# Kernel tuning notes

Measured on AMD Instinct MI355X. Metric: run time of the kernel, lower is better.

Reference implementation:

```python
import jax, jax.numpy as jnp
import numpy as np
from jax import lax

RATES = (2, 3, 5, 9)
C_IN = 64
B, H, W = 4, 128, 128


def conv2d(x, w, b, dilation):
    # x: [B,C,H,W], w: [O,I,3,3]; padding=dilation keeps spatial size
    y = lax.conv_general_dilated(
        x, w, window_strides=(1, 1),
        padding=[(dilation, dilation), (dilation, dilation)],
        rhs_dilation=(dilation, dilation),
        dimension_numbers=('NCHW', 'OIHW', 'NCHW'))
    return y + b[None, :, None, None]


def bilinear_sample(x, py, px):
    # x: [B,C,H,W]; py,px: [B,K,H,W] float sampling positions; zeros outside
    Hh, Ww = x.shape[-2], x.shape[-1]
    y0 = jnp.floor(py)
    x0 = jnp.floor(px)
    wy1 = py - y0
    wx1 = px - x0
    wy0 = 1.0 - wy1
    wx0 = 1.0 - wx1

    def gather(yi, xi):
        valid = (yi >= 0) & (yi < Hh) & (xi >= 0) & (xi < Ww)
        yc = jnp.clip(yi, 0, Hh - 1).astype(jnp.int32)
        xc = jnp.clip(xi, 0, Ww - 1).astype(jnp.int32)
        # per-batch fancy gather: [C,K,H,W]
        vals = jax.vmap(lambda im, yy, xx: im[:, yy, xx])(x, yc, xc)
        return vals * valid[:, None].astype(x.dtype)

    out = (gather(y0, x0) * (wy0 * wx0)[:, None]
           + gather(y0, x0 + 1) * (wy0 * wx1)[:, None]
           + gather(y0 + 1, x0) * (wy1 * wx0)[:, None]
           + gather(y0 + 1, x0 + 1) * (wy1 * wx1)[:, None])
    return out  # [B,C,K,H,W]


def deform_conv(x, offset, weight, dilation):
    # offset: [B,18,H,W] = (dy,dx) per kernel point; weight: [O,C,3,3]
    b, c, h, w = x.shape
    K = 9
    off = offset.reshape(b, K, 2, h, w)
    dy, dx = off[:, :, 0], off[:, :, 1]
    ky = jnp.repeat((jnp.arange(3) - 1) * dilation, 3).astype(x.dtype)  # [9]
    kx = jnp.tile((jnp.arange(3) - 1) * dilation, 3).astype(x.dtype)
    hh = jnp.arange(h, dtype=x.dtype)[None, None, :, None]
    ww = jnp.arange(w, dtype=x.dtype)[None, None, None, :]
    py = hh + ky[None, :, None, None] + dy
    px = ww + kx[None, :, None, None] + dx
    sampled = bilinear_sample(x, py, px)  # [B,C,K,H,W]
    w9 = weight.reshape(weight.shape[0], c, K)
    return jnp.einsum('bckhw,ock->bohw', sampled, w9)


def setup_inputs() -> dict:
    key = jax.random.key(0)
    ks = jax.random.split(key, 8)
    s = 0.05
    return {
        'x': jax.random.normal(ks[0], (B, C_IN, H, W), jnp.float32),
        'dw': jax.random.normal(ks[1], (4, C_IN, C_IN, 3, 3), jnp.float32) * s,
        'ow': jax.random.normal(ks[2], (4, 18, C_IN, 3, 3), jnp.float32) * s,
        'ob': jax.random.normal(ks[3], (4, 18), jnp.float32) * s,
        'se_w1': jax.random.normal(ks[4], (C_IN, 4 * C_IN), jnp.float32) * s,
        'se_b1': jax.random.normal(ks[5], (C_IN,), jnp.float32) * s,
        'se_w2': jax.random.normal(ks[6], (4 * C_IN, C_IN), jnp.float32) * s,
        'se_b2': jax.random.normal(ks[7], (4 * C_IN,), jnp.float32) * s,
    }


def reference(x, dw, ow, ob, se_w1, se_b1, se_w2, se_b2):
    b, c, h, w = x.shape
    outs = []
    for i in range(4):
        j = (i - 1) % 4  # faithful to `self.offsets[i - 1]` in the source
        off = jax.nn.relu(conv2d(x, ow[j], ob[j], RATES[j]))
        outs.append(deform_conv(x, off, dw[i], RATES[i]))
    cat = jnp.concatenate(outs, axis=1)  # [B,4C,H,W]
    # SENet on concatenated features
    g = cat.mean(axis=(2, 3))  # [B,4C]
    h1 = jax.nn.relu(g @ se_w1.T + se_b1)
    s = jax.nn.sigmoid(h1 @ se_w2.T + se_b2)  # [B,4C]
    gated = (1.0 + s)[:, :, None, None] * cat
    fused = gated.reshape(b, 4, c, h, w).sum(axis=1)  # sum over the 4 stages
    return x + fused
```

## Files before the change

### kernel.cpp

```cpp
#include <hip/hip_runtime.h>
#include <hip/hip_bf16.h>
#include <math.h>

#define BATCH 4
#define CIN 64
#define HH 128
#define WW 128
#define HWP (HH*WW)

#define OFF_OFF   0
#define CAT_OFF   4718592
#define XHWC_OFF  (CAT_OFF + 8388608)
#define WTH_OFF   (XHWC_OFF + 2097152)
#define OWH_OFF   (WTH_OFF + 73728)
#define G_OFF     (OWH_OFF + 36864)
#define SCALE_OFF (G_OFF + 1024)

typedef _Float16 h16x2 __attribute__((ext_vector_type(2)));
typedef _Float16 h16x8 __attribute__((ext_vector_type(8)));
typedef float    f32x4 __attribute__((ext_vector_type(4)));

union h8view { h16x8 v8; h16x2 v2[4]; };

__device__ __forceinline__ int rate_of(int i) {
    return (i == 0) ? 2 : (i == 1) ? 3 : (i == 2) ? 5 : 9;
}

__global__ __launch_bounds__(256) void prep_kernel(
    const float* __restrict__ dw, const float* __restrict__ ow,
    _Float16* __restrict__ wth, _Float16* __restrict__ owh)
{
    int idx = blockIdx.x * 256 + threadIdx.x;
    if (idx < 147456) {
        int c = idx & 63;
        int k = (idx >> 6) % 9;
        int r = idx / 576;
        int o = r & 63;
        int i = r >> 6;
        wth[idx] = (_Float16)dw[((i * 64 + o) * 64 + c) * 9 + k];
        return;
    }
    int idx2 = idx - 147456;
    if (idx2 < 73728) {
        int c = idx2 & 63;
        int r = idx2 >> 6;
        int o = r & 31;
        int r2 = r >> 5;
        int tap = r2 % 9;
        int j = r2 / 9;
        owh[idx2] = (o < 18) ? (_Float16)ow[((j * 18 + o) * 64 + c) * 9 + tap]
                             : (_Float16)0.f;
    }
}

__global__ __launch_bounds__(256) void xhwc_kernel(
    const float* __restrict__ x, _Float16* __restrict__ xhwc)
{
    const int t  = threadIdx.x;
    const int b  = blockIdx.y;
    const int p0 = blockIdx.x * 64;
    const int px = t & 63;
    const int cO = t >> 6;

    const float* xb = x + (size_t)b * CIN * HWP + p0 + px;
    _Float16* xh = xhwc + ((size_t)b * HWP + p0 + px) * 64;

#pragma unroll
    for (int g = 0; g < 2; ++g) {
        const int cb = cO * 8 + g * 32;
        h16x8 v;
#pragma unroll
        for (int cj = 0; cj < 8; ++cj)
            v[cj] = (_Float16)xb[(size_t)(cb + cj) * HWP];
        *(h16x8*)(xh + cb) = v;
    }
}

__global__ __launch_bounds__(256) void offset_mfma_kernel(
    const _Float16* __restrict__ xhwc, const _Float16* __restrict__ owh,
    const float* __restrict__ ob, float* __restrict__ off)
{
    __shared__ __align__(16) _Float16 S2[64][72];

    const int t  = threadIdx.x;
    const int z  = blockIdx.y;
    const int j  = z >> 2, b = z & 3;
    const int d  = rate_of(j);
    const int p0 = blockIdx.x * 64;
    const int ph = p0 >> 7;
    const int cb0 = p0 & 127;

    const int wv = t >> 6, lane = t & 63;
    const int nl = lane & 15, quad = lane >> 4;

    const _Float16* xh = xhwc + (size_t)b * HWP * 64;

    f32x4 acc[2];
    acc[0] = (f32x4){0.f, 0.f, 0.f, 0.f};
    acc[1] = (f32x4){0.f, 0.f, 0.f, 0.f};

    for (int k = 0; k < 9; ++k) {
        const int iy = k / 3, ix = k % 3;
        const int ys = ph + (iy - 1) * d;
        const bool rowok = (unsigned)ys < (unsigned)HH;

        if (k) __syncthreads();

#pragma unroll
        for (int q = 0; q < 2; ++q) {
            const int task = q * 256 + t;
            const int px = task >> 3, chunk = task & 7;
            const int xs = cb0 + px + (ix - 1) * d;
            h16x8 v = {};
            if (rowok && (unsigned)xs < (unsigned)WW)
                v = *(const h16x8*)(xh + ((size_t)(ys * WW + xs)) * 64 + chunk * 8);
            *(h16x8*)&S2[px][chunk * 8] = v;
        }
        __syncthreads();

#pragma unroll
        for (int q2 = 0; q2 < 2; ++q2) {
            h16x8 a = *(const h16x8*)&S2[wv * 16 + nl][q2 * 32 + quad * 8];
#pragma unroll
            for (int nt = 0; nt < 2; ++nt) {
                const _Float16* brow = owh
                    + ((size_t)((j * 9 + k) * 32 + nt * 16 + nl)) * 64;
                h16x8 bf = *(const h16x8*)&brow[q2 * 32 + quad * 8];
                acc[nt] = __builtin_amdgcn_mfma_f32_16x16x32_f16(a, bf, acc[nt], 0, 0, 0);
            }
        }
    }

    float* op = off + (size_t)z * 18 * HWP + p0;
#pragma unroll
    for (int nt = 0; nt < 2; ++nt) {
        const int o = nt * 16 + nl;
        if (o < 18) {
            const float bias = ob[j * 18 + o];
#pragma unroll
            for (int r = 0; r < 4; ++r) {
                const int pxl = wv * 16 + quad * 4 + r;
                op[(size_t)o * HWP + pxl] = fmaxf(acc[nt][r] + bias, 0.f);
            }
        }
    }
}

__global__ __launch_bounds__(256) void deform_mfma_kernel(
    const _Float16* __restrict__ xhwc, const _Float16* __restrict__ wth,
    const float* __restrict__ off, _Float16* __restrict__ cat)
{
    __shared__ __align__(16) _Float16 S[128][72];

    const int t  = threadIdx.x;
    const int z  = blockIdx.y;
    const int i  = z >> 2, b = z & 3;
    const int d  = rate_of(i);
    const int j  = (i + 3) & 3;
    const int ty = blockIdx.x >> 1;
    const int tx = blockIdx.x & 1;

    const int chunk = t & 7;
    const int pxb   = t >> 3;

    const int wv = t >> 6, lane = t & 63;
    const int nl = lane & 15, quad = lane >> 4;

    const _Float16* xh = xhwc + (size_t)b * HWP * 64;
    const float* offb = off + ((size_t)(j * 4 + b) * 18) * HWP;

    f32x4 acc[8];
#pragma unroll
    for (int a = 0; a < 8; ++a) acc[a] = (f32x4){0.f, 0.f, 0.f, 0.f};

    for (int k = 0; k < 9; ++k) {
        const int iy = k / 3, ix = k % 3;

        if (k) __syncthreads();

#pragma unroll
        for (int it = 0; it < 4; ++it) {
            const int psub = it * 32 + pxb;
            const int sly = psub >> 6, slx = psub & 63;
            const int ph = ty * 2 + sly, pw = tx * 64 + slx;
            const int pg = ph * WW + pw;

            float dy = offb[(2 * k) * HWP + pg];
            float dx = offb[(2 * k + 1) * HWP + pg];
            float py = (float)(ph + (iy - 1) * d) + dy;
            float px = (float)(pw + (ix - 1) * d) + dx;
            float fy0 = floorf(py), fx0 = floorf(px);
            float wy1 = py - fy0, wx1 = px - fx0;
            float wy0 = 1.f - wy1, wx0 = 1.f - wx1;
            int y0 = (int)fy0, x0 = (int)fx0;
            int y1 = y0 + 1,  x1 = x0 + 1;
            bool vy0 = (unsigned)y0 < (unsigned)HH, vy1 = (unsigned)y1 < (unsigned)HH;
            bool vx0 = (unsigned)x0 < (unsigned)WW, vx1 = (unsigned)x1 < (unsigned)WW;
            int yc0 = min(max(y0, 0), HH - 1), yc1 = min(max(y1, 0), HH - 1);
            int xc0 = min(max(x0, 0), WW - 1), xc1 = min(max(x1, 0), WW - 1);
            float w00 = (vy0 && vx0) ? wy0 * wx0 : 0.f;
            float w01 = (vy0 && vx1) ? wy0 * wx1 : 0.f;
            float w10 = (vy1 && vx0) ? wy1 * wx0 : 0.f;
            float w11 = (vy1 && vx1) ? wy1 * wx1 : 0.f;

            const _Float16 h00 = (_Float16)w00, h01 = (_Float16)w01;
            const _Float16 h10 = (_Float16)w10, h11 = (_Float16)w11;
            const h16x2 w00p = {h00, h00}, w01p = {h01, h01};
            const h16x2 w10p = {h10, h10}, w11p = {h11, h11};

            const int cb = chunk * 8;
            h8view u00, u01, u10, u11, outv;
            u00.v8 = *(const h16x8*)(xh + (size_t)(yc0 * WW + xc0) * 64 + cb);
            u01.v8 = *(const h16x8*)(xh + (size_t)(yc0 * WW + xc1) * 64 + cb);
            u10.v8 = *(const h16x8*)(xh + (size_t)(yc1 * WW + xc0) * 64 + cb);
            u11.v8 = *(const h16x8*)(xh + (size_t)(yc1 * WW + xc1) * 64 + cb);
#pragma unroll
            for (int pp = 0; pp < 4; ++pp) {
                h16x2 r = u00.v2[pp] * w00p + u01.v2[pp] * w01p
                        + u10.v2[pp] * w10p + u11.v2[pp] * w11p;
                outv.v2[pp] = r;
            }
            *(h16x8*)&S[psub][cb] = outv.v8;
        }
        __syncthreads();

#pragma unroll
        for (int q2 = 0; q2 < 2; ++q2) {
            h16x8 b0 = *(const h16x8*)&S[wv * 32 + nl][q2 * 32 + quad * 8];
            h16x8 b1 = *(const h16x8*)&S[wv * 32 + 16 + nl][q2 * 32 + quad * 8];
#pragma unroll
            for (int mt = 0; mt < 4; ++mt) {
                const _Float16* wrow = wth
                    + ((size_t)((i * 64 + mt * 16 + nl) * 9 + k)) * 64;
                h16x8 a = *(const h16x8*)&wrow[q2 * 32 + quad * 8];
                acc[mt * 2 + 0] = __builtin_amdgcn_mfma_f32_16x16x32_f16(a, b0, acc[mt * 2 + 0], 0, 0, 0);
                acc[mt * 2 + 1] = __builtin_amdgcn_mfma_f32_16x16x32_f16(a, b1, acc[mt * 2 + 1], 0, 0, 0);
            }
        }
    }

#pragma unroll
    for (int mt = 0; mt < 4; ++mt) {
#pragma unroll
        for (int nt = 0; nt < 2; ++nt) {
            const int psub = wv * 32 + nt * 16 + nl;
            const int prow = ty * 2 + (psub >> 6);
            const int pcol = tx * 64 + (psub & 63);
            _Float16* cp = cat
                + ((size_t)(b * 256 + i * 64 + mt * 16 + quad * 4)) * HWP
                + prow * WW + pcol;
            const f32x4 v = acc[mt * 2 + nt];
#pragma unroll
            for (int r = 0; r < 4; ++r)
                cp[(size_t)r * HWP] = (_Float16)v[r];
        }
    }
}

__global__ __launch_bounds__(256) void reduce_kernel(
    const _Float16* __restrict__ cat, float* __restrict__ g)
{
    const int bc = blockIdx.x;
    const _Float16* p = cat + (size_t)bc * HWP;
    float s = 0.f;
#pragma unroll
    for (int q = 0; q < 8; ++q) {
        h16x8 v8 = *(const h16x8*)(p + q * 2048 + threadIdx.x * 8);
#pragma unroll
        for (int e = 0; e < 8; ++e) s += (float)v8[e];
    }
#pragma unroll
    for (int o = 32; o > 0; o >>= 1) s += __shfl_down(s, o, 64);
    __shared__ float ls[4];
    if ((threadIdx.x & 63) == 0) ls[threadIdx.x >> 6] = s;
    __syncthreads();
    if (threadIdx.x == 0) {
        g[bc] = (ls[0] + ls[1] + ls[2] + ls[3]) * (1.f / (float)HWP);
    }
}

__global__ __launch_bounds__(256) void se_kernel(
    const float* __restrict__ g,  const float* __restrict__ w1,
    const float* __restrict__ b1, const float* __restrict__ w2,
    const float* __restrict__ b2, float* __restrict__ scale)
{
    __shared__ float gs[1024];
    __shared__ float h1s[256];
    const int t = threadIdx.x;
#pragma unroll
    for (int q = 0; q < 4; ++q) gs[q * 256 + t] = g[q * 256 + t];
    __syncthreads();
    {
        int b = t >> 6, o = t & 63;
        float a = b1[o];
        for (int c = 0; c < 256; ++c)
            a = fmaf(gs[b * 256 + c], w1[o * 256 + c], a);
        h1s[t] = fmaxf(a, 0.f);
    }
    __syncthreads();
#pragma unroll
    for (int q = 0; q < 4; ++q) {
        int idx = q * 256 + t;
        int b = idx >> 8, cc = idx & 255;
        float a = b2[cc];
#pragma unroll 8
        for (int o = 0; o < 64; ++o)
            a = fmaf(h1s[b * 64 + o], w2[cc * 64 + o], a);
        scale[idx] = 1.f + 1.f / (1.f + expf(-a));
    }
}

__global__ __launch_bounds__(256) void final_kernel(
    const float* __restrict__ x, const _Float16* __restrict__ cat,
    const float* __restrict__ scale, float* __restrict__ out)
{
    const int gid = blockIdx.x;
    const int p = (gid & 63) * 256 + threadIdx.x;
    const int c = (gid >> 6) & 63;
    const int b = gid >> 12;
    const float s0 = scale[b * 256 + c];
    const float s1 = scale[b * 256 + 64 + c];
    const float s2 = scale[b * 256 + 128 + c];
    const float s3 = scale[b * 256 + 192 + c];
    const _Float16* cb = cat + ((size_t)(b * 256 + c)) * HWP + p;
    float v = x[(size_t)(b * 64 + c) * HWP + p];
    v = fmaf(s0, (float)cb[0 * 64 * HWP], v);
    v = fmaf(s1, (float)cb[1 * 64 * HWP], v);
    v = fmaf(s2, (float)cb[2 * 64 * HWP], v);
    v = fmaf(s3, (float)cb[3 * 64 * HWP], v);
    out[(size_t)(b * 64 + c) * HWP + p] = v;
}

extern "C" void kernel_launch(void* const* d_in, const int* in_sizes, int n_in,
                              void* d_out, int out_size, void* d_ws, size_t ws_size,
                              hipStream_t stream) {
    const float* x  = (const float*)d_in[0];
    const float* dw = (const float*)d_in[1];
    const float* ow = (const float*)d_in[2];
    const float* ob = (const float*)d_in[3];
    const float* w1 = (const float*)d_in[4];
    const float* b1 = (const float*)d_in[5];
    const float* w2 = (const float*)d_in[6];
    const float* b2 = (const float*)d_in[7];
    float* out = (float*)d_out;
    float* ws  = (float*)d_ws;

    float* OFF      = ws + OFF_OFF;
    _Float16* CAT   = (_Float16*)(ws + CAT_OFF);
    _Float16* XHWC  = (_Float16*)(ws + XHWC_OFF);
    _Float16* WTH   = (_Float16*)(ws + WTH_OFF);
    _Float16* OWH   = (_Float16*)(ws + OWH_OFF);
    float* G        = ws + G_OFF;
    float* SCALE    = ws + SCALE_OFF;

    prep_kernel<<<864, 256, 0, stream>>>(dw, ow, WTH, OWH);
    xhwc_kernel<<<dim3(256, 4), 256, 0, stream>>>(x, XHWC);
    offset_mfma_kernel<<<dim3(256, 16), 256, 0, stream>>>(XHWC, OWH, ob, OFF);
    deform_mfma_kernel<<<dim3(128, 16), 256, 0, stream>>>(XHWC, WTH, OFF, CAT);
    reduce_kernel<<<1024, 256, 0, stream>>>(CAT, G);
    se_kernel<<<1, 256, 0, stream>>>(G, w1, b1, w2, b2, SCALE);
    final_kernel<<<16384, 256, 0, stream>>>(x, CAT, SCALE, out);
}
```

Measured before the change: 312.9 us.

## Double-buffer LDS staging in offset and deform MFMA kernels with register prefetch

Both the offset convolution kernel and the deformable convolution kernel now use two LDS buffers. The global loads (or bilinear gathers) for the next kernel tap are issued into registers before the MFMA work on the current tap and written to the other buffer afterwards, leaving one barrier per tap instead of two. The deform kernel also prefetches offsets two taps ahead and hoists the pixel index math. This is meant to hide gather latency behind MFMA, at the cost of doubled LDS and many more live registers (16 h16x8 values plus weights), which may reduce occupancy or cause spills.

```diff
diff --git a/kernel.cpp b/kernel.cpp
--- a/kernel.cpp
+++ b/kernel.cpp
@@ -80,7 +80,7 @@
     const _Float16* __restrict__ xhwc, const _Float16* __restrict__ owh,
     const float* __restrict__ ob, float* __restrict__ off)
 {
-    __shared__ __align__(16) _Float16 S2[64][72];
+    __shared__ __align__(16) _Float16 S2[2][64][72];
 
     const int t  = threadIdx.x;
     const int z  = blockIdx.y;
@@ -99,28 +99,42 @@
     acc[0] = (f32x4){0.f, 0.f, 0.f, 0.f};
     acc[1] = (f32x4){0.f, 0.f, 0.f, 0.f};
 
-    for (int k = 0; k < 9; ++k) {
-        const int iy = k / 3, ix = k % 3;
+    h16x8 v[2];
+
+    auto stage_load = [&](int kk) {
+        const int iy = kk / 3, ix = kk % 3;
         const int ys = ph + (iy - 1) * d;
         const bool rowok = (unsigned)ys < (unsigned)HH;
-
-        if (k) __syncthreads();
-
 #pragma unroll
         for (int q = 0; q < 2; ++q) {
             const int task = q * 256 + t;
-            const int px = task >> 3, chunk = task & 7;
+            const int px = task >> 3, ch = task & 7;
             const int xs = cb0 + px + (ix - 1) * d;
-            h16x8 v = {};
+            h16x8 vv = {};
             if (rowok && (unsigned)xs < (unsigned)WW)
-                v = *(const h16x8*)(xh + ((size_t)(ys * WW + xs)) * 64 + chunk * 8);
-            *(h16x8*)&S2[px][chunk * 8] = v;
-        }
-        __syncthreads();
+                vv = *(const h16x8*)(xh + ((size_t)(ys * WW + xs)) * 64 + ch * 8);
+            v[q] = vv;
+        }
+    };
+    auto stage_store = [&](int buf) {
+#pragma unroll
+        for (int q = 0; q < 2; ++q) {
+            const int task = q * 256 + t;
+            const int px = task >> 3, ch = task & 7;
+            *(h16x8*)&S2[buf][px][ch * 8] = v[q];
+        }
+    };
+
+    stage_load(0);
+    stage_store(0);
+    __syncthreads();
+
+    for (int k = 0; k < 9; ++k) {
+        if (k < 8) stage_load(k + 1);
 
 #pragma unroll
         for (int q2 = 0; q2 < 2; ++q2) {
-            h16x8 a = *(const h16x8*)&S2[wv * 16 + nl][q2 * 32 + quad * 8];
+            h16x8 a = *(const h16x8*)&S2[k & 1][wv * 16 + nl][q2 * 32 + quad * 8];
 #pragma unroll
             for (int nt = 0; nt < 2; ++nt) {
                 const _Float16* brow = owh
@@ -129,6 +143,9 @@
                 acc[nt] = __builtin_amdgcn_mfma_f32_16x16x32_f16(a, bf, acc[nt], 0, 0, 0);
             }
         }
+
+        if (k < 8) stage_store((k + 1) & 1);
+        __syncthreads();
     }
 
     float* op = off + (size_t)z * 18 * HWP + p0;
@@ -150,7 +167,7 @@
     const _Float16* __restrict__ xhwc, const _Float16* __restrict__ wth,
     const float* __restrict__ off, _Float16* __restrict__ cat)
 {
-    __shared__ __align__(16) _Float16 S[128][72];
+    __shared__ __align__(16) _Float16 S[2][128][72];
 
     const int t  = threadIdx.x;
     const int z  = blockIdx.y;
@@ -162,6 +179,7 @@
 
     const int chunk = t & 7;
     const int pxb   = t >> 3;
+    const int cb    = chunk * 8;
 
     const int wv = t >> 6, lane = t & 63;
     const int nl = lane & 15, quad = lane >> 4;
@@ -169,26 +187,30 @@
     const _Float16* xh = xhwc + (size_t)b * HWP * 64;
     const float* offb = off + ((size_t)(j * 4 + b) * 18) * HWP;
 
+    int phv[4], pwv[4], pgv[4];
+#pragma unroll
+    for (int it = 0; it < 4; ++it) {
+        const int psub = it * 32 + pxb;
+        phv[it] = ty * 2 + (psub >> 6);
+        pwv[it] = tx * 64 + (psub & 63);
+        pgv[it] = phv[it] * WW + pwv[it];
+    }
+
     f32x4 acc[8];
 #pragma unroll
     for (int a = 0; a < 8; ++a) acc[a] = (f32x4){0.f, 0.f, 0.f, 0.f};
 
-    for (int k = 0; k < 9; ++k) {
-        const int iy = k / 3, ix = k % 3;
-
-        if (k) __syncthreads();
-
+    h8view u[4][4];
+    h16x2  wp[4][4];
+    float  ocy[4], ocx[4];
+    float  ony[4], onx[4];
+
+    auto gather = [&](int kk) {
+        const int iy = kk / 3, ix = kk % 3;
 #pragma unroll
         for (int it = 0; it < 4; ++it) {
-            const int psub = it * 32 + pxb;
-            const int sly = psub >> 6, slx = psub & 63;
-            const int ph = ty * 2 + sly, pw = tx * 64 + slx;
-            const int pg = ph * WW + pw;
-
-            float dy = offb[(2 * k) * HWP + pg];
-            float dx = offb[(2 * k + 1) * HWP + pg];
-            float py = (float)(ph + (iy - 1) * d) + dy;
-            float px = (float)(pw + (ix - 1) * d) + dx;
+            float py = (float)(phv[it] + (iy - 1) * d) + ocy[it];
+            float px = (float)(pwv[it] + (ix - 1) * d) + ocx[it];
             float fy0 = floorf(py), fx0 = floorf(px);
             float wy1 = py - fy0, wx1 = px - fx0;
             float wy0 = 1.f - wy1, wx0 = 1.f - wx1;
@@ -202,32 +224,61 @@
             float w01 = (vy0 && vx1) ? wy0 * wx1 : 0.f;
             float w10 = (vy1 && vx0) ? wy1 * wx0 : 0.f;
             float w11 = (vy1 && vx1) ? wy1 * wx1 : 0.f;
-
             const _Float16 h00 = (_Float16)w00, h01 = (_Float16)w01;
             const _Float16 h10 = (_Float16)w10, h11 = (_Float16)w11;
-            const h16x2 w00p = {h00, h00}, w01p = {h01, h01};
-            const h16x2 w10p = {h10, h10}, w11p = {h11, h11};
-
-            const int cb = chunk * 8;
-            h8view u00, u01, u10, u11, outv;
-            u00.v8 = *(const h16x8*)(xh + (size_t)(yc0 * WW + xc0) * 64 + cb);
-            u01.v8 = *(const h16x8*)(xh + (size_t)(yc0 * WW + xc1) * 64 + cb);
-            u10.v8 = *(const h16x8*)(xh + (size_t)(yc1 * WW + xc0) * 64 + cb);
-            u11.v8 = *(const h16x8*)(xh + (size_t)(yc1 * WW + xc1) * 64 + cb);
-#pragma unroll
-            for (int pp = 0; pp < 4; ++pp) {
-                h16x2 r = u00.v2[pp] * w00p + u01.v2[pp] * w01p
-                        + u10.v2[pp] * w10p + u11.v2[pp] * w11p;
-                outv.v2[pp] = r;
+            wp[it][0] = (h16x2){h00, h00};
+            wp[it][1] = (h16x2){h01, h01};
+            wp[it][2] = (h16x2){h10, h10};
+            wp[it][3] = (h16x2){h11, h11};
+            u[it][0].v8 = *(const h16x8*)(xh + (size_t)(yc0 * WW + xc0) * 64 + cb);
+            u[it][1].v8 = *(const h16x8*)(xh + (size_t)(yc0 * WW + xc1) * 64 + cb);
+            u[it][2].v8 = *(const h16x8*)(xh + (size_t)(yc1 * WW + xc0) * 64 + cb);
+            u[it][3].v8 = *(const h16x8*)(xh + (size_t)(yc1 * WW + xc1) * 64 + cb);
+        }
+    };
+
+    auto blendstore = [&](int buf) {
+#pragma unroll
+        for (int it = 0; it < 4; ++it) {
+            h8view outv;
+#pragma unroll
+            for (int pp = 0; pp < 4; ++pp)
+                outv.v2[pp] = u[it][0].v2[pp] * wp[it][0] + u[it][1].v2[pp] * wp[it][1]
+                            + u[it][2].v2[pp] * wp[it][2] + u[it][3].v2[pp] * wp[it][3];
+            *(h16x8*)&S[buf][it * 32 + pxb][cb] = outv.v8;
+        }
+    };
+
+#pragma unroll
+    for (int it = 0; it < 4; ++it) {
+        ocy[it] = offb[0 * HWP + pgv[it]];
+        ocx[it] = offb[1 * HWP + pgv[it]];
+    }
+    gather(0);
+    blendstore(0);
+#pragma unroll
+    for (int it = 0; it < 4; ++it) {
+        ocy[it] = offb[2 * HWP + pgv[it]];
+        ocx[it] = offb[3 * HWP + pgv[it]];
+    }
+    __syncthreads();
+
+    for (int k = 0; k < 9; ++k) {
+        if (k < 8) {
+            gather(k + 1);
+            if (k < 7) {
+#pragma unroll
+                for (int it = 0; it < 4; ++it) {
+                    ony[it] = offb[(2 * (k + 2)) * HWP + pgv[it]];
+                    onx[it] = offb[(2 * (k + 2) + 1) * HWP + pgv[it]];
+                }
             }
-            *(h16x8*)&S[psub][cb] = outv.v8;
-        }
-        __syncthreads();
+        }
 
 #pragma unroll
         for (int q2 = 0; q2 < 2; ++q2) {
-            h16x8 b0 = *(const h16x8*)&S[wv * 32 + nl][q2 * 32 + quad * 8];
-            h16x8 b1 = *(const h16x8*)&S[wv * 32 + 16 + nl][q2 * 32 + quad * 8];
+            h16x8 b0 = *(const h16x8*)&S[k & 1][wv * 32 + nl][q2 * 32 + quad * 8];
+            h16x8 b1 = *(const h16x8*)&S[k & 1][wv * 32 + 16 + nl][q2 * 32 + quad * 8];
 #pragma unroll
             for (int mt = 0; mt < 4; ++mt) {
                 const _Float16* wrow = wth
@@ -237,6 +288,13 @@
                 acc[mt * 2 + 1] = __builtin_amdgcn_mfma_f32_16x16x32_f16(a, b1, acc[mt * 2 + 1], 0, 0, 0);
             }
         }
+
+        if (k < 8) {
+            blendstore((k + 1) & 1);
+#pragma unroll
+            for (int it = 0; it < 4; ++it) { ocy[it] = ony[it]; ocx[it] = onx[it]; }
+        }
+        __syncthreads();
     }
 
 #pragma unroll
```

After: 305.4 us. -2.4%, faster.

## Merge prep kernels, stage offset-conv row halos, store offsets as fp16, fuse pooling

Applied to the files above, without the earlier changes.

Merges the weight-prep and NHWC conversion kernels into one launch that also zeroes the pooling buffer. The offset convolution now stages one padded input row per kernel row in shared memory, reused by three taps with register prefetch, instead of reloading for each of nine taps. Offsets are written as interleaved fp16 (dy,dx) pairs, halving offset traffic. The separate mean-reduction kernel is removed: per-channel sums are reduced in the deform kernel and accumulated with atomics. This costs some offset precision and adds atomic contention and ordering nondeterminism.

```diff
diff --git a/kernel.cpp b/kernel.cpp
--- a/kernel.cpp
+++ b/kernel.cpp
@@ -26,61 +26,67 @@
     return (i == 0) ? 2 : (i == 1) ? 3 : (i == 2) ? 5 : 9;
 }
 
-__global__ __launch_bounds__(256) void prep_kernel(
-    const float* __restrict__ dw, const float* __restrict__ ow,
-    _Float16* __restrict__ wth, _Float16* __restrict__ owh)
-{
-    int idx = blockIdx.x * 256 + threadIdx.x;
-    if (idx < 147456) {
-        int c = idx & 63;
-        int k = (idx >> 6) % 9;
-        int r = idx / 576;
-        int o = r & 63;
-        int i = r >> 6;
-        wth[idx] = (_Float16)dw[((i * 64 + o) * 64 + c) * 9 + k];
+__global__ __launch_bounds__(256) void prep_all_kernel(
+    const float* __restrict__ x,  const float* __restrict__ dw,
+    const float* __restrict__ ow, _Float16* __restrict__ wth,
+    _Float16* __restrict__ owh,   _Float16* __restrict__ xhwc,
+    float* __restrict__ g)
+{
+    const int bx = blockIdx.x;
+    const int t  = threadIdx.x;
+
+    if (bx < 864) {
+        int idx = bx * 256 + t;
+        if (idx < 147456) {
+            int c = idx & 63;
+            int k = (idx >> 6) % 9;
+            int r = idx / 576;
+            int o = r & 63;
+            int i = r >> 6;
+            wth[idx] = (_Float16)dw[((i * 64 + o) * 64 + c) * 9 + k];
+            return;
+        }
+        int idx2 = idx - 147456;
+        if (idx2 < 73728) {
+            int c = idx2 & 63;
+            int r = idx2 >> 6;
+            int o = r & 31;
+            int r2 = r >> 5;
+            int tap = r2 % 9;
+            int j = r2 / 9;
+            owh[idx2] = (o < 18) ? (_Float16)ow[((j * 18 + o) * 64 + c) * 9 + tap]
+                                 : (_Float16)0.f;
+        }
         return;
     }
-    int idx2 = idx - 147456;
-    if (idx2 < 73728) {
-        int c = idx2 & 63;
-        int r = idx2 >> 6;
-        int o = r & 31;
-        int r2 = r >> 5;
-        int tap = r2 % 9;
-        int j = r2 / 9;
-        owh[idx2] = (o < 18) ? (_Float16)ow[((j * 18 + o) * 64 + c) * 9 + tap]
-                             : (_Float16)0.f;
-    }
-}
-
-__global__ __launch_bounds__(256) void xhwc_kernel(
-    const float* __restrict__ x, _Float16* __restrict__ xhwc)
-{
-    const int t  = threadIdx.x;
-    const int b  = blockIdx.y;
-    const int p0 = blockIdx.x * 64;
-    const int px = t & 63;
-    const int cO = t >> 6;
-
-    const float* xb = x + (size_t)b * CIN * HWP + p0 + px;
-    _Float16* xh = xhwc + ((size_t)b * HWP + p0 + px) * 64;
-
-#pragma unroll
-    for (int g = 0; g < 2; ++g) {
-        const int cb = cO * 8 + g * 32;
-        h16x8 v;
-#pragma unroll
-        for (int cj = 0; cj < 8; ++cj)
-            v[cj] = (_Float16)xb[(size_t)(cb + cj) * HWP];
-        *(h16x8*)(xh + cb) = v;
-    }
+    if (bx < 1888) {
+        const int tb = bx - 864;
+        const int b  = tb >> 8;
+        const int p0 = (tb & 255) * 64;
+        const int px = t & 63;
+        const int cO = t >> 6;
+        const float* xb = x + (size_t)b * CIN * HWP + p0 + px;
+        _Float16* xh = xhwc + ((size_t)b * HWP + p0 + px) * 64;
+#pragma unroll
+        for (int gq = 0; gq < 2; ++gq) {
+            const int cb = cO * 8 + gq * 32;
+            h16x8 v;
+#pragma unroll
+            for (int cj = 0; cj < 8; ++cj)
+                v[cj] = (_Float16)xb[(size_t)(cb + cj) * HWP];
+            *(h16x8*)(xh + cb) = v;
+        }
+        return;
+    }
+#pragma unroll
+    for (int q = 0; q < 4; ++q) g[q * 256 + t] = 0.f;
 }
 
 __global__ __launch_bounds__(256) void offset_mfma_kernel(
     const _Float16* __restrict__ xhwc, const _Float16* __restrict__ owh,
-    const float* __restrict__ ob, float* __restrict__ off)
-{
-    __shared__ __align__(16) _Float16 S2[64][72];
+    const float* __restrict__ ob, _Float16* __restrict__ offh)
+{
+    __shared__ __align__(16) _Float16 S2[82][72];
 
     const int t  = threadIdx.x;
     const int z  = blockIdx.y;
@@ -95,52 +101,83 @@
 
     const _Float16* xh = xhwc + (size_t)b * HWP * 64;
 
+    const int width = 64 + 2 * d;
+    const int ntask = width * 8;
+
     f32x4 acc[2];
     acc[0] = (f32x4){0.f, 0.f, 0.f, 0.f};
     acc[1] = (f32x4){0.f, 0.f, 0.f, 0.f};
 
-    for (int k = 0; k < 9; ++k) {
-        const int iy = k / 3, ix = k % 3;
-        const int ys = ph + (iy - 1) * d;
+    h16x8 sv[3];
+
+    auto stage_load = [&](int g) {
+        const int ys = ph + (g - 1) * d;
         const bool rowok = (unsigned)ys < (unsigned)HH;
-
-        if (k) __syncthreads();
-
-#pragma unroll
-        for (int q = 0; q < 2; ++q) {
+#pragma unroll
+        for (int q = 0; q < 3; ++q) {
             const int task = q * 256 + t;
-            const int px = task >> 3, chunk = task & 7;
-            const int xs = cb0 + px + (ix - 1) * d;
-            h16x8 v = {};
-            if (rowok && (unsigned)xs < (unsigned)WW)
-                v = *(const h16x8*)(xh + ((size_t)(ys * WW + xs)) * 64 + chunk * 8);
-            *(h16x8*)&S2[px][chunk * 8] = v;
-        }
+            h16x8 vv = {};
+            if (task < ntask) {
+                const int sp = task >> 3, ch = task & 7;
+                const int xs = cb0 - d + sp;
+                if (rowok && (unsigned)xs < (unsigned)WW)
+                    vv = *(const h16x8*)(xh + ((size_t)(ys * WW + xs)) * 64 + ch * 8);
+            }
+            sv[q] = vv;
+        }
+    };
+    auto stage_store = [&]() {
+#pragma unroll
+        for (int q = 0; q < 3; ++q) {
+            const int task = q * 256 + t;
+            if (task < ntask) {
+                const int sp = task >> 3, ch = task & 7;
+                *(h16x8*)&S2[sp][ch * 8] = sv[q];
+            }
+        }
+    };
+
+    stage_load(0);
+    stage_store();
+    __syncthreads();
+
+    for (int g = 0; g < 3; ++g) {
+        if (g < 2) stage_load(g + 1);
+
+#pragma unroll
+        for (int ix = 0; ix < 3; ++ix) {
+            const int k = g * 3 + ix;
+#pragma unroll
+            for (int q2 = 0; q2 < 2; ++q2) {
+                h16x8 a = *(const h16x8*)&S2[wv * 16 + nl + ix * d][q2 * 32 + quad * 8];
+#pragma unroll
+                for (int nt = 0; nt < 2; ++nt) {
+                    const _Float16* brow = owh
+                        + ((size_t)((j * 9 + k) * 32 + nt * 16 + nl)) * 64;
+                    h16x8 bf = *(const h16x8*)&brow[q2 * 32 + quad * 8];
+                    acc[nt] = __builtin_amdgcn_mfma_f32_16x16x32_f16(a, bf, acc[nt], 0, 0, 0);
+                }
+            }
+        }
+
         __syncthreads();
-
-#pragma unroll
-        for (int q2 = 0; q2 < 2; ++q2) {
-            h16x8 a = *(const h16x8*)&S2[wv * 16 + nl][q2 * 32 + quad * 8];
-#pragma unroll
-            for (int nt = 0; nt < 2; ++nt) {
-                const _Float16* brow = owh
-                    + ((size_t)((j * 9 + k) * 32 + nt * 16 + nl)) * 64;
-                h16x8 bf = *(const h16x8*)&brow[q2 * 32 + quad * 8];
-                acc[nt] = __builtin_amdgcn_mfma_f32_16x16x32_f16(a, bf, acc[nt], 0, 0, 0);
-            }
-        }
-    }
-
-    float* op = off + (size_t)z * 18 * HWP + p0;
+        if (g < 2) stage_store();
+        __syncthreads();
+    }
+
+    _Float16* op = offh + (size_t)z * 9 * HWP * 2;
 #pragma unroll
     for (int nt = 0; nt < 2; ++nt) {
         const int o = nt * 16 + nl;
         if (o < 18) {
             const float bias = ob[j * 18 + o];
+            const int k  = o >> 1;
+            const int lo = o & 1;
 #pragma unroll
             for (int r = 0; r < 4; ++r) {
                 const int pxl = wv * 16 + quad * 4 + r;
-                op[(size_t)o * HWP + pxl] = fmaxf(acc[nt][r] + bias, 0.f);
+                op[((size_t)k * HWP + p0 + pxl) * 2 + lo] =
+                    (_Float16)fmaxf(acc[nt][r] + bias, 0.f);
             }
         }
     }
@@ -148,7 +185,8 @@
 
 __global__ __launch_bounds__(256) void deform_mfma_kernel(
     const _Float16* __restrict__ xhwc, const _Float16* __restrict__ wth,
-    const float* __restrict__ off, _Float16* __restrict__ cat)
+    const _Float16* __restrict__ offh, _Float16* __restrict__ cat,
+    float* __restrict__ g)
 {
     __shared__ __align__(16) _Float16 S[128][72];
 
@@ -162,12 +200,13 @@
 
     const int chunk = t & 7;
     const int pxb   = t >> 3;
+    const int cb    = chunk * 8;
 
     const int wv = t >> 6, lane = t & 63;
     const int nl = lane & 15, quad = lane >> 4;
 
     const _Float16* xh = xhwc + (size_t)b * HWP * 64;
-    const float* offb = off + ((size_t)(j * 4 + b) * 18) * HWP;
+    const _Float16* offb = offh + (size_t)(j * 4 + b) * 9 * HWP * 2;
 
     f32x4 acc[8];
 #pragma unroll
@@ -185,8 +224,9 @@
             const int ph = ty * 2 + sly, pw = tx * 64 + slx;
             const int pg = ph * WW + pw;
 
-            float dy = offb[(2 * k) * HWP + pg];
-            float dx = offb[(2 * k + 1) * HWP + pg];
+            h16x2 od = *(const h16x2*)&offb[((size_t)k * HWP + pg) * 2];
+            float dy = (float)od[0];
+            float dx = (float)od[1];
             float py = (float)(ph + (iy - 1) * d) + dy;
             float px = (float)(pw + (ix - 1) * d) + dx;
             float fy0 = floorf(py), fx0 = floorf(px);
@@ -208,7 +248,6 @@
             const h16x2 w00p = {h00, h00}, w01p = {h01, h01};
             const h16x2 w10p = {h10, h10}, w11p = {h11, h11};
 
-            const int cb = chunk * 8;
             h8view u00, u01, u10, u11, outv;
             u00.v8 = *(const h16x8*)(xh + (size_t)(yc0 * WW + xc0) * 64 + cb);
             u01.v8 = *(const h16x8*)(xh + (size_t)(yc0 * WW + xc1) * 64 + cb);
@@ -255,27 +294,18 @@
                 cp[(size_t)r * HWP] = (_Float16)v[r];
         }
     }
-}
-
-__global__ __launch_bounds__(256) void reduce_kernel(
-    const _Float16* __restrict__ cat, float* __restrict__ g)
-{
-    const int bc = blockIdx.x;
-    const _Float16* p = cat + (size_t)bc * HWP;
-    float s = 0.f;
-#pragma unroll
-    for (int q = 0; q < 8; ++q) {
-        h16x8 v8 = *(const h16x8*)(p + q * 2048 + threadIdx.x * 8);
-#pragma unroll
-        for (int e = 0; e < 8; ++e) s += (float)v8[e];
-    }
-#pragma unroll
-    for (int o = 32; o > 0; o >>= 1) s += __shfl_down(s, o, 64);
-    __shared__ float ls[4];
-    if ((threadIdx.x & 63) == 0) ls[threadIdx.x >> 6] = s;
-    __syncthreads();
-    if (threadIdx.x == 0) {
-        g[bc] = (ls[0] + ls[1] + ls[2] + ls[3]) * (1.f / (float)HWP);
+
+#pragma unroll
+    for (int mt = 0; mt < 4; ++mt) {
+#pragma unroll
+        for (int r = 0; r < 4; ++r) {
+            float s = acc[mt * 2 + 0][r] + acc[mt * 2 + 1][r];
+#pragma unroll
+            for (int o2 = 1; o2 < 16; o2 <<= 1)
+                s += __shfl_xor(s, o2, 64);
+            if (nl == 0)
+                atomicAdd(&g[b * 256 + i * 64 + mt * 16 + quad * 4 + r], s);
+        }
     }
 }
 
@@ -288,7 +318,8 @@
     __shared__ float h1s[256];
     const int t = threadIdx.x;
 #pragma unroll
-    for (int q = 0; q < 4; ++q) gs[q * 256 + t] = g[q * 256 + t];
+    for (int q = 0; q < 4; ++q)
+        gs[q * 256 + t] = g[q * 256 + t] * (1.f / (float)HWP);
     __syncthreads();
     {
         int b = t >> 6, o = t & 63;
@@ -345,7 +376,7 @@
     float* out = (float*)d_out;
     float* ws  = (float*)d_ws;
 
-    float* OFF      = ws + OFF_OFF;
+    _Float16* OFFH  = (_Float16*)(ws + OFF_OFF);
     _Float16* CAT   = (_Float16*)(ws + CAT_OFF);
     _Float16* XHWC  = (_Float16*)(ws + XHWC_OFF);
     _Float16* WTH   = (_Float16*)(ws + WTH_OFF);
@@ -353,11 +384,9 @@
     float* G        = ws + G_OFF;
     float* SCALE    = ws + SCALE_OFF;
 
-    prep_kernel<<<864, 256, 0, stream>>>(dw, ow, WTH, OWH);
-    xhwc_kernel<<<dim3(256, 4), 256, 0, stream>>>(x, XHWC);
-    offset_mfma_kernel<<<dim3(256, 16), 256, 0, stream>>>(XHWC, OWH, ob, OFF);
-    deform_mfma_kernel<<<dim3(128, 16), 256, 0, stream>>>(XHWC, WTH, OFF, CAT);
-    reduce_kernel<<<1024, 256, 0, stream>>>(CAT, G);
+    prep_all_kernel<<<1889, 256, 0, stream>>>(x, dw, ow, WTH, OWH, XHWC, G);
+    offset_mfma_kernel<<<dim3(256, 16), 256, 0, stream>>>(XHWC, OWH, ob, OFFH);
+    deform_mfma_kernel<<<dim3(128, 16), 256, 0, stream>>>(XHWC, WTH, OFFH, CAT, G);
     se_kernel<<<1, 256, 0, stream>>>(G, w1, b1, w2, b2, SCALE);
     final_kernel<<<16384, 256, 0, stream>>>(x, CAT, SCALE, out);
 }
```

Result: slower. 412.5 us (+31.9%).
